# Performance work log

Hardware: AMD Instinct MI355X
Metric: run time of the kernel (lower is better)

The kernel has to match this reference:

```python
import jax, jax.numpy as jnp
import numpy as np

N = 50000
IN_DIM, HID_DIM, OUT_DIM = 16, 64, 32


def setup_inputs() -> dict:
    key = jax.random.key(0)
    k1, k2, k3, k4, k5 = jax.random.split(key, 5)
    x = jax.random.normal(k1, (N, IN_DIM), dtype=jnp.float32)
    edge_index = jax.random.randint(k2, (2, 800000), 0, N, dtype=jnp.int64)
    # GCNConv weights (glorot-ish scale) and biases
    W1 = jax.random.normal(k3, (IN_DIM, HID_DIM), dtype=jnp.float32) / np.sqrt(IN_DIM)
    b1 = jnp.zeros((HID_DIM,), dtype=jnp.float32)
    W2 = jax.random.normal(k4, (HID_DIM, OUT_DIM), dtype=jnp.float32) / np.sqrt(HID_DIM)
    b2 = jnpplus = jnp.zeros((OUT_DIM,), dtype=jnp.float32)
    return {"x": x, "edge_index": edge_index, "W1": W1, "b1": b1, "W2": W2, "b2": b2}


def _gcn_conv(x, src, dst, norm, W, b, num_nodes):
    # PyG GCNConv: h = X W; out[d] = sum_e norm_e * h[src_e]; out += b
    h = x @ W                                   # [N, D_out] small GEMM
    msgs = h[src] * norm[:, None]               # [E+N, D_out] gather (memory-bound)
    out = jax.ops.segment_sum(msgs, dst, num_segments=num_nodes)  # scatter-add
    return out + b


def reference(x, edge_index, W1, b1, W2, b2):
    num_nodes = x.shape[0]
    # add self-loops (PyG GCNConv default add_self_loops=True)
    loops = jnp.arange(num_nodes, dtype=edge_index.dtype)
    src = jnp.concatenate([edge_index[0], loops])
    dst = jnp.concatenate([edge_index[1], loops])
    # symmetric normalization D^{-1/2} (A+I) D^{-1/2}, degree over dst
    deg = jax.ops.segment_sum(jnp.ones_like(src, dtype=x.dtype), dst, num_segments=num_nodes)
    dinv = jnp.where(deg > 0, jax.lax.rsqrt(deg), 0.0)
    norm = dinv[src] * dinv[dst]                # [E+N]

    h = _gcn_conv(x, src, dst, norm, W1, b1, num_nodes)
    h = jax.nn.relu(h)
    out = _gcn_conv(h, src, dst, norm, W2, b2, num_nodes)
    return out
```

## Files before the change

### kernel.cpp

```cpp
#include <hip/hip_runtime.h>
#include <hip/hip_fp16.h>

#define IN_DIM  16
#define HID_DIM 64
#define OUT_DIM 32

#define CAP   8192
#define EPB   1024
#define EPT   4
#define CONVB 64
#define PBT   1024

__device__ __forceinline__ int detect_is64(const void* edges) {
    const int* w = (const int*)edges;
    int is64 = 1;
    #pragma unroll
    for (int i = 0; i < 16; ++i) is64 &= (w[2 * i + 1] == 0);
    return is64;
}

__device__ __forceinline__ long long edge_at(const void* edges, int is64, long long i) {
    if (is64) return ((const long long*)edges)[i];
    return (long long)((const int*)edges)[i];
}

__device__ __forceinline__ int block_incl_scan(int v, int t, int* wsum) {
    int lane = t & 63, w = t >> 6;
    int s = v;
    #pragma unroll
    for (int d = 1; d < 64; d <<= 1) {
        int u = __shfl_up(s, d, 64);
        if (lane >= d) s += u;
    }
    if (lane == 63) wsum[w] = s;
    __syncthreads();
    int add = 0;
    #pragma unroll
    for (int i = 0; i < 4; ++i)
        if (i < w) add += wsum[i];
    return s + add;
}

__global__ __launch_bounds__(256) void k_partA(const void* edges, int* gcur,
                                               unsigned int* gpart, int nbuk, long long E,
                                               const float* __restrict__ x,
                                               __half* __restrict__ xh,
                                               long long xElems, int nblkA) {
    if (blockIdx.x >= nblkA) {
        const float4* x4 = (const float4*)x;
        uint2* outp = (uint2*)xh;
        long long n4 = xElems >> 2;
        for (long long i = (long long)(blockIdx.x - nblkA) * 256 + threadIdx.x;
             i < n4; i += (long long)CONVB * 256) {
            float4 v = x4[i];
            __half2 a = __floats2half2_rn(v.x, v.y);
            __half2 b = __floats2half2_rn(v.z, v.w);
            outp[i] = make_uint2(*(unsigned int*)&a, *(unsigned int*)&b);
        }
        return;
    }

    __shared__ unsigned int staged[EPB];
    __shared__ int hcnt[256], hoff[256], hcur[256];
    __shared__ int wsum[4];
    __shared__ int s64s;
    int t = threadIdx.x;
    if (t == 0) s64s = detect_is64(edges);
    hcnt[t] = 0;
    __syncthreads();
    int is64 = s64s;

    long long e0 = (long long)blockIdx.x * EPB;
    unsigned int rs[EPT], rd[EPT];
    int nval = 0;
    #pragma unroll
    for (int k = 0; k < EPT; ++k) {
        long long e = e0 + t + k * 256;
        if (e < E) {
            rs[k] = (unsigned int)edge_at(edges, is64, e);
            rd[k] = (unsigned int)edge_at(edges, is64, E + e);
            atomicAdd(&hcnt[rd[k] >> 8], 1);
            nval = k + 1;
        }
    }
    __syncthreads();

    int v = hcnt[t];
    int incl = block_incl_scan(v, t, wsum);
    int excl = incl - v;
    hoff[t] = excl;
    hcur[t] = excl;
    __syncthreads();

    #pragma unroll
    for (int k = 0; k < EPT; ++k) {
        if (k < nval) {
            int p = atomicAdd(&hcur[rd[k] >> 8], 1);
            staged[p] = rs[k] | ((rd[k] & 255u) << 16);
        }
    }
    __syncthreads();

    if (t < nbuk) {
        int c = hcnt[t];
        if (c > 0) {
            int base = atomicAdd(&gcur[t], c);
            int o = hoff[t];
            for (int k = 0; k < c; ++k) {
                int idx = base + k;
                if (idx < CAP) gpart[(size_t)t * CAP + idx] = staged[o + k];
            }
        }
    }
}

__global__ __launch_bounds__(PBT) void k_partB(const int* __restrict__ gcur,
                                               const unsigned int* __restrict__ gpart,
                                               unsigned short* __restrict__ csr,
                                               int* __restrict__ offs,
                                               float* __restrict__ dinv,
                                               int nbuk, int N) {
    __shared__ unsigned int   ebuf[CAP];
    __shared__ unsigned short sbuf[CAP];
    __shared__ int bscan[256];
    __shared__ int hcnt[256], hcur[256];
    __shared__ int wsum[4];
    int t = threadIdx.x;
    int lane = t & 63, wv = t >> 6;
    int b = blockIdx.x;

    int bc = (t < 256 && t < nbuk) ? min(gcur[t], CAP) : 0;
    if (t < 256) hcnt[t] = 0;
    int s = bc;
    #pragma unroll
    for (int d = 1; d < 64; d <<= 1) {
        int u = __shfl_up(s, d, 64);
        if (lane >= d) s += u;
    }
    if (t < 256 && lane == 63) wsum[wv] = s;
    __syncthreads();
    if (t < 256) {
        int add = 0;
        #pragma unroll
        for (int i = 0; i < 4; ++i)
            if (i < wv) add += wsum[i];
        bscan[t] = s + add;
    }
    __syncthreads();
    int base = (b == 0) ? 0 : bscan[b - 1];
    int cnt  = bscan[b] - base;

    for (int i = t; i < cnt; i += PBT) ebuf[i] = gpart[(size_t)b * CAP + i];
    __syncthreads();
    for (int i = t; i < cnt; i += PBT) atomicAdd(&hcnt[(ebuf[i] >> 16) & 255u], 1);
    __syncthreads();

    int v = (t < 256) ? hcnt[t] : 0;
    s = v;
    #pragma unroll
    for (int d = 1; d < 64; d <<= 1) {
        int u = __shfl_up(s, d, 64);
        if (lane >= d) s += u;
    }
    if (t < 256 && lane == 63) wsum[wv] = s;
    __syncthreads();
    if (t < 256) {
        int add = 0;
        #pragma unroll
        for (int i = 0; i < 4; ++i)
            if (i < wv) add += wsum[i];
        int excl = (s + add) - v;
        hcur[t] = excl;
        int node = b * 256 + t;
        if (node < N) {
            offs[node] = base + excl;
            dinv[node] = rsqrtf((float)v + 1.0f);
        }
    }
    if (b == nbuk - 1 && t == 0) offs[N] = bscan[nbuk - 1];
    __syncthreads();

    for (int i = t; i < cnt; i += PBT) {
        unsigned int e = ebuf[i];
        int p = atomicAdd(&hcur[(e >> 16) & 255u], 1);
        sbuf[p] = (unsigned short)(e & 0xffffu);
    }
    __syncthreads();
    for (int i = t; i < cnt; i += PBT) csr[base + i] = sbuf[i];
}

#define ASTR 17
#define H1S  68
__global__ __launch_bounds__(256, 6) void k_agg1g(
    const __half* __restrict__ xh, const float* __restrict__ dinv,
    const int* __restrict__ offs, const unsigned short* __restrict__ csr,
    const float* __restrict__ W1, const float* __restrict__ b1,
    const float* __restrict__ W2, __half* __restrict__ h2, int N)
{
    __shared__ __align__(16) float W1s[IN_DIM * HID_DIM];
    __shared__ __align__(16) float W2s[HID_DIM * OUT_DIM];
    __shared__ float b1s[HID_DIM];
    __shared__ __align__(16) float aggs[16 * ASTR];
    __shared__ __align__(16) float h1s[16 * H1S];

    int tid = threadIdx.x;
    int lane = tid & 63;
    int g = lane >> 4, sub = lane & 15;
    int comp = sub >> 3;
    int way  = sub & 7;
    int nl   = (tid >> 6) * 4 + g;
    int node = blockIdx.x * 16 + nl;

    float di = 0.f;
    int start = 0, end = 0;
    if (node < N) {
        di = dinv[node];
        start = offs[node];
        end = offs[node + 1];
    }

    for (int i = tid; i < IN_DIM * HID_DIM; i += 256) W1s[i] = W1[i];
    for (int i = tid; i < HID_DIM * OUT_DIM; i += 256) W2s[i] = W2[i];
    if (tid < HID_DIM) b1s[tid] = b1[tid];

    float acc[8] = {0.f, 0.f, 0.f, 0.f, 0.f, 0.f, 0.f, 0.f};
    if (node < N) {
        const uint4* x2 = (const uint4*)xh;
        if (way == 0) {
            uint4 r = x2[(size_t)node * 2 + comp];
            const __half2* hp = (const __half2*)&r;
            #pragma unroll
            for (int c = 0; c < 4; ++c) {
                float2 f = __half22float2(hp[c]);
                acc[c * 2]     = di * f.x;
                acc[c * 2 + 1] = di * f.y;
            }
        }
        int j = start + way;
        for (; j + 8 < end; j += 16) {
            int s0 = csr[j], s1 = csr[j + 8];
            float w0 = dinv[s0], w1 = dinv[s1];
            uint4 r0 = x2[(size_t)s0 * 2 + comp];
            uint4 r1 = x2[(size_t)s1 * 2 + comp];
            const __half2* hp0 = (const __half2*)&r0;
            const __half2* hp1 = (const __half2*)&r1;
            #pragma unroll
            for (int c = 0; c < 4; ++c) {
                float2 f0 = __half22float2(hp0[c]);
                float2 f1 = __half22float2(hp1[c]);
                acc[c * 2]     += w0 * f0.x + w1 * f1.x;
                acc[c * 2 + 1] += w0 * f0.y + w1 * f1.y;
            }
        }
        if (j < end) {
            int s = csr[j];
            float w = dinv[s];
            uint4 r = x2[(size_t)s * 2 + comp];
            const __half2* hp = (const __half2*)&r;
            #pragma unroll
            for (int c = 0; c < 4; ++c) {
                float2 f = __half22float2(hp[c]);
                acc[c * 2]     += w * f.x;
                acc[c * 2 + 1] += w * f.y;
            }
        }
        #pragma unroll
        for (int m = 1; m <= 4; m <<= 1) {
            #pragma unroll
            for (int c = 0; c < 8; ++c) acc[c] += __shfl_xor(acc[c], m, 64);
        }
    }
    if (way == 0) {
        #pragma unroll
        for (int c = 0; c < 8; ++c) aggs[nl * ASTR + comp * 8 + c] = di * acc[c];
    }
    __syncthreads();

    int nl2 = tid >> 4, q = tid & 15;

    float a1[4];
    #pragma unroll
    for (int c = 0; c < 4; ++c) a1[c] = b1s[q * 4 + c];
    #pragma unroll
    for (int k = 0; k < IN_DIM; ++k) {
        float a = aggs[nl2 * ASTR + k];
        float4 w = *(const float4*)&W1s[k * HID_DIM + q * 4];
        a1[0] += a * w.x; a1[1] += a * w.y; a1[2] += a * w.z; a1[3] += a * w.w;
    }
    *(float4*)&h1s[nl2 * H1S + q * 4] =
        make_float4(fmaxf(a1[0], 0.f), fmaxf(a1[1], 0.f),
                    fmaxf(a1[2], 0.f), fmaxf(a1[3], 0.f));
    __syncthreads();

    float a2x = 0.f, a2y = 0.f;
    const float4* h1row = (const float4*)&h1s[nl2 * H1S];
    #pragma unroll
    for (int k4 = 0; k4 < 16; ++k4) {
        float4 hv = h1row[k4];
        const float* wb = &W2s[(k4 * 4) * OUT_DIM + q * 2];
        float2 w0 = *(const float2*)(wb);
        float2 w1 = *(const float2*)(wb + OUT_DIM);
        float2 w2 = *(const float2*)(wb + 2 * OUT_DIM);
        float2 w3 = *(const float2*)(wb + 3 * OUT_DIM);
        a2x += hv.x * w0.x + hv.y * w1.x + hv.z * w2.x + hv.w * w3.x;
        a2y += hv.x * w0.y + hv.y * w1.y + hv.z * w2.y + hv.w * w3.y;
    }
    int gn = blockIdx.x * 16 + nl2;
    if (gn < N) {
        __half2 p = __floats2half2_rn(a2x, a2y);
        ((unsigned int*)h2)[(size_t)gn * 16 + q] = *(unsigned int*)&p;
    }
}

__global__ __launch_bounds__(256, 8) void k_agg2(
    const __half* __restrict__ h2, const float* __restrict__ dinv,
    const int* __restrict__ offs, const unsigned short* __restrict__ csr,
    const float* __restrict__ b2, float* __restrict__ out, int N)
{
    int gtid = blockIdx.x * 256 + threadIdx.x;
    int lane = gtid & 63;
    int g = lane >> 4, sub = lane & 15;
    int comp = sub & 3, way = sub >> 2;
    int node = (gtid >> 6) * 4 + g;
    if (node >= N) return;
    const uint4* h24 = (const uint4*)h2;
    float di = dinv[node];
    int start = offs[node], end = offs[node + 1];
    float acc[8] = {0.f, 0.f, 0.f, 0.f, 0.f, 0.f, 0.f, 0.f};
    if (way == 0) {
        uint4 r = h24[(size_t)node * 4 + comp];
        const __half2* hp = (const __half2*)&r;
        #pragma unroll
        for (int c = 0; c < 4; ++c) {
            float2 f = __half22float2(hp[c]);
            acc[c * 2]     = di * f.x;
            acc[c * 2 + 1] = di * f.y;
        }
    }
    int j = start + way;
    for (; j + 4 < end; j += 8) {
        int s0 = csr[j], s1 = csr[j + 4];
        float w0 = dinv[s0], w1 = dinv[s1];
        uint4 r0 = h24[(size_t)s0 * 4 + comp];
        uint4 r1 = h24[(size_t)s1 * 4 + comp];
        const __half2* hp0 = (const __half2*)&r0;
        const __half2* hp1 = (const __half2*)&r1;
        #pragma unroll
        for (int c = 0; c < 4; ++c) {
            float2 f0 = __half22float2(hp0[c]);
            float2 f1 = __half22float2(hp1[c]);
            acc[c * 2]     += w0 * f0.x + w1 * f1.x;
            acc[c * 2 + 1] += w0 * f0.y + w1 * f1.y;
        }
    }
    if (j < end) {
        int s = csr[j];
        float w = dinv[s];
        uint4 r = h24[(size_t)s * 4 + comp];
        const __half2* hp = (const __half2*)&r;
        #pragma unroll
        for (int c = 0; c < 4; ++c) {
            float2 f = __half22float2(hp[c]);
            acc[c * 2]     += w * f.x;
            acc[c * 2 + 1] += w * f.y;
        }
    }
    #pragma unroll
    for (int m = 4; m <= 8; m <<= 1) {
        #pragma unroll
        for (int c = 0; c < 8; ++c) acc[c] += __shfl_xor(acc[c], m, 64);
    }
    if (way == 0) {
        const float4* b24 = (const float4*)b2;
        float4 bb0 = b24[comp * 2], bb1 = b24[comp * 2 + 1];
        float4* out4 = (float4*)out;
        out4[(size_t)node * 8 + comp * 2 + 0] =
            make_float4(di * acc[0] + bb0.x, di * acc[1] + bb0.y,
                        di * acc[2] + bb0.z, di * acc[3] + bb0.w);
        out4[(size_t)node * 8 + comp * 2 + 1] =
            make_float4(di * acc[4] + bb1.x, di * acc[5] + bb1.y,
                        di * acc[6] + bb1.z, di * acc[7] + bb1.w);
    }
}

extern "C" void kernel_launch(void* const* d_in, const int* in_sizes, int n_in,
                              void* d_out, int out_size, void* d_ws, size_t ws_size,
                              hipStream_t stream) {
    const float* x     = (const float*)d_in[0];
    const void*  edges = d_in[1];
    const float* W1    = (const float*)d_in[2];
    const float* b1    = (const float*)d_in[3];
    const float* W2    = (const float*)d_in[4];
    const float* b2    = (const float*)d_in[5];
    float* out = (float*)d_out;

    const int       N = in_sizes[0] / IN_DIM;
    const long long E = in_sizes[1] / 2;
    const int    NBUK = (N + 255) >> 8;
    const int   NBLKA = (int)((E + EPB - 1) / EPB);

    unsigned short* csr   = (unsigned short*)d_ws;
    unsigned int*   gpart = (unsigned int*)(csr + ((E + 7) & ~7LL));
    __half* xh       = (__half*)(gpart + (size_t)NBUK * CAP);
    __half* h2       = (__half*)(xh + (size_t)IN_DIM * N);
    float*  dinv     = (float*)(h2 + (size_t)OUT_DIM * N);
    int*    offs     = (int*)(dinv + N);
    int*    gcur     = offs + N + 1;

    const int B = 256;
    hipMemsetAsync(gcur, 0, (size_t)NBUK * sizeof(int), stream);
    k_partA<<<NBLKA + CONVB, B, 0, stream>>>(edges, gcur, gpart, NBUK, E,
                                             x, xh, (long long)N * IN_DIM, NBLKA);
    k_partB<<<NBUK, PBT, 0, stream>>>(gcur, gpart, csr, offs, dinv, NBUK, N);

    k_agg1g<<<(N + 15) / 16, B, 0, stream>>>(xh, dinv, offs, csr,
                                             W1, b1, W2, h2, N);
    k_agg2<<<(N + 15) / 16, B, 0, stream>>>(h2, dinv, offs, csr, b2, out, N);
}
```

Baseline: 143.6 us.

## Store per-block bucket runs contiguously and gather them in partB via histogram

partA now writes its whole locally bucket-sorted edge chunk contiguously and records per-block bucket counts and offsets, instead of doing serialized per-thread scattered writes into global buckets reserved by atomics. A small scan kernel computes the bucket bases, and partB gathers each bucket's runs from every producer block using the per-block histograms. Edges per block rise to 3328 so the number of producer blocks fits the 256-thread scan in partB. The aim is coalesced writes in partA and no per-bucket serial copy loop, at the cost of an extra launch and many short strided reads in partB.

```diff
diff --git a/kernel.cpp b/kernel.cpp
--- a/kernel.cpp
+++ b/kernel.cpp
@@ -5,11 +5,11 @@
 #define HID_DIM 64
 #define OUT_DIM 32
 
-#define CAP   8192
-#define EPB   1024
-#define EPT   4
+#define EPB   3328
+#define EPT   13
 #define CONVB 64
 #define PBT   1024
+#define BCAP  8192
 
 __device__ __forceinline__ int detect_is64(const void* edges) {
     const int* w = (const int*)edges;
@@ -41,8 +41,12 @@
     return s + add;
 }
 
-__global__ __launch_bounds__(256) void k_partA(const void* edges, int* gcur,
-                                               unsigned int* gpart, int nbuk, long long E,
+__global__ __launch_bounds__(256) void k_partA(const void* edges,
+                                               unsigned int* __restrict__ gpart,
+                                               int* __restrict__ H,
+                                               int* __restrict__ Hoff,
+                                               int* __restrict__ tot,
+                                               int nbuk, long long E,
                                                const float* __restrict__ x,
                                                __half* __restrict__ xh,
                                                long long xElems, int nblkA) {
@@ -61,9 +65,9 @@
     }
 
     __shared__ unsigned int staged[EPB];
-    __shared__ int hcnt[256], hoff[256], hcur[256];
+    __shared__ int hcnt[256], hoffs[256], hcur[256];
     __shared__ int wsum[4];
-    __shared__ int s64s;
+    __shared__ int s64s, sTot;
     int t = threadIdx.x;
     if (t == 0) s64s = detect_is64(edges);
     hcnt[t] = 0;
@@ -88,8 +92,9 @@
     int v = hcnt[t];
     int incl = block_incl_scan(v, t, wsum);
     int excl = incl - v;
-    hoff[t] = excl;
+    hoffs[t] = excl;
     hcur[t] = excl;
+    if (t == 255) sTot = incl;
     __syncthreads();
 
     #pragma unroll
@@ -101,37 +106,55 @@
     }
     __syncthreads();
 
+    int nvt = sTot;
+    for (int i = t; i < nvt; i += 256)
+        gpart[(size_t)blockIdx.x * EPB + i] = staged[i];
+
     if (t < nbuk) {
         int c = hcnt[t];
-        if (c > 0) {
-            int base = atomicAdd(&gcur[t], c);
-            int o = hoff[t];
-            for (int k = 0; k < c; ++k) {
-                int idx = base + k;
-                if (idx < CAP) gpart[(size_t)t * CAP + idx] = staged[o + k];
-            }
-        }
-    }
-}
-
-__global__ __launch_bounds__(PBT) void k_partB(const int* __restrict__ gcur,
-                                               const unsigned int* __restrict__ gpart,
+        H[blockIdx.x * nbuk + t]    = c;
+        Hoff[blockIdx.x * nbuk + t] = hoffs[t];
+        if (c > 0) atomicAdd(&tot[t], c);
+    }
+}
+
+__global__ __launch_bounds__(256) void k_scan(const int* __restrict__ tot,
+                                              int* __restrict__ base, int nbuk) {
+    __shared__ int wsum[4];
+    int t = threadIdx.x;
+    int v = (t < nbuk) ? tot[t] : 0;
+    int incl = block_incl_scan(v, t, wsum);
+    if (t < nbuk) base[t] = incl - v;
+    if (t == nbuk - 1) base[nbuk] = incl;
+}
+
+__global__ __launch_bounds__(PBT) void k_partB(const unsigned int* __restrict__ gpart,
+                                               const int* __restrict__ H,
+                                               const int* __restrict__ Hoff,
+                                               const int* __restrict__ base,
                                                unsigned short* __restrict__ csr,
                                                int* __restrict__ offs,
                                                float* __restrict__ dinv,
-                                               int nbuk, int N) {
-    __shared__ unsigned int   ebuf[CAP];
-    __shared__ unsigned short sbuf[CAP];
-    __shared__ int bscan[256];
+                                               int nbuk, int nblkA, int N) {
+    __shared__ unsigned int   ebuf[BCAP];
+    __shared__ unsigned short sbuf[BCAP];
+    __shared__ int runS[256], runC[256], runD[256];
     __shared__ int hcnt[256], hcur[256];
     __shared__ int wsum[4];
+    __shared__ int sTot;
     int t = threadIdx.x;
     int lane = t & 63, wv = t >> 6;
     int b = blockIdx.x;
 
-    int bc = (t < 256 && t < nbuk) ? min(gcur[t], CAP) : 0;
-    if (t < 256) hcnt[t] = 0;
-    int s = bc;
+    int c_i = 0, s_i = 0;
+    if (t < 256) {
+        if (t < nblkA) {
+            c_i = H[t * nbuk + b];
+            s_i = Hoff[t * nbuk + b];
+        }
+        hcnt[t] = 0;
+    }
+    int s = c_i;
     #pragma unroll
     for (int d = 1; d < 64; d <<= 1) {
         int u = __shfl_up(s, d, 64);
@@ -144,14 +167,23 @@
         #pragma unroll
         for (int i = 0; i < 4; ++i)
             if (i < wv) add += wsum[i];
-        bscan[t] = s + add;
-    }
-    __syncthreads();
-    int base = (b == 0) ? 0 : bscan[b - 1];
-    int cnt  = bscan[b] - base;
-
-    for (int i = t; i < cnt; i += PBT) ebuf[i] = gpart[(size_t)b * CAP + i];
-    __syncthreads();
+        int incl = s + add;
+        runD[t] = incl - c_i;
+        runC[t] = c_i;
+        runS[t] = t * EPB + s_i;
+        if (t == 255) sTot = incl;
+    }
+    __syncthreads();
+    int bbase = base[b];
+    int cnt   = sTot;
+
+    for (int r = wv; r < nblkA; r += (PBT / 64)) {
+        int c = runC[r], d0 = runD[r], s0 = runS[r];
+        for (int o = lane; o < c; o += 64)
+            ebuf[d0 + o] = gpart[s0 + o];
+    }
+    __syncthreads();
+
     for (int i = t; i < cnt; i += PBT) atomicAdd(&hcnt[(ebuf[i] >> 16) & 255u], 1);
     __syncthreads();
 
@@ -173,11 +205,11 @@
         hcur[t] = excl;
         int node = b * 256 + t;
         if (node < N) {
-            offs[node] = base + excl;
+            offs[node] = bbase + excl;
             dinv[node] = rsqrtf((float)v + 1.0f);
         }
     }
-    if (b == nbuk - 1 && t == 0) offs[N] = bscan[nbuk - 1];
+    if (b == nbuk - 1 && t == 0) offs[N] = bbase + cnt;
     __syncthreads();
 
     for (int i = t; i < cnt; i += PBT) {
@@ -186,7 +218,7 @@
         sbuf[p] = (unsigned short)(e & 0xffffu);
     }
     __syncthreads();
-    for (int i = t; i < cnt; i += PBT) csr[base + i] = sbuf[i];
+    for (int i = t; i < cnt; i += PBT) csr[bbase + i] = sbuf[i];
 }
 
 #define ASTR 17
@@ -401,17 +433,22 @@
 
     unsigned short* csr   = (unsigned short*)d_ws;
     unsigned int*   gpart = (unsigned int*)(csr + ((E + 7) & ~7LL));
-    __half* xh       = (__half*)(gpart + (size_t)NBUK * CAP);
-    __half* h2       = (__half*)(xh + (size_t)IN_DIM * N);
-    float*  dinv     = (float*)(h2 + (size_t)OUT_DIM * N);
-    int*    offs     = (int*)(dinv + N);
-    int*    gcur     = offs + N + 1;
+    int*    H    = (int*)(gpart + (size_t)NBLKA * EPB);
+    int*    Hoff = H + (size_t)NBLKA * NBUK;
+    int*    tot  = Hoff + (size_t)NBLKA * NBUK;
+    int*    base = tot + NBUK;
+    __half* xh   = (__half*)(base + NBUK + 1);
+    __half* h2   = (__half*)(xh + (size_t)IN_DIM * N);
+    float*  dinv = (float*)(h2 + (size_t)OUT_DIM * N);
+    int*    offs = (int*)(dinv + N);
 
     const int B = 256;
-    hipMemsetAsync(gcur, 0, (size_t)NBUK * sizeof(int), stream);
-    k_partA<<<NBLKA + CONVB, B, 0, stream>>>(edges, gcur, gpart, NBUK, E,
+    hipMemsetAsync(tot, 0, (size_t)NBUK * sizeof(int), stream);
+    k_partA<<<NBLKA + CONVB, B, 0, stream>>>(edges, gpart, H, Hoff, tot, NBUK, E,
                                              x, xh, (long long)N * IN_DIM, NBLKA);
-    k_partB<<<NBUK, PBT, 0, stream>>>(gcur, gpart, csr, offs, dinv, NBUK, N);
+    k_scan<<<1, B, 0, stream>>>(tot, base, NBUK);
+    k_partB<<<NBUK, PBT, 0, stream>>>(gpart, H, Hoff, base, csr, offs, dinv,
+                                      NBUK, NBLKA, N);
 
     k_agg1g<<<(N + 15) / 16, B, 0, stream>>>(xh, dinv, offs, csr,
                                              W1, b1, W2, h2, N);
```

Measured after the change: 134.2 us. -6.6%, faster.

## Enlarge partition blocks to 1024 threads and 3328 edges per block

Applied to the files above, without the earlier changes.

Each partition block of k_partA now uses 1024 threads and handles 3328 edges instead of 256 threads and 1024 edges, and the conversion tail drops from 64 to 16 blocks. The aim is to cut the number of blocks doing global atomic reservations per bucket and to write larger contiguous runs per bucket into gpart. The block scan is rewritten so only the first 256 threads hold histogram bins. The cost is a larger staged shared buffer and fewer, bigger blocks, which may lower occupancy and parallelism.

```diff
diff --git a/kernel.cpp b/kernel.cpp
--- a/kernel.cpp
+++ b/kernel.cpp
@@ -6,9 +6,10 @@
 #define OUT_DIM 32
 
 #define CAP   8192
-#define EPB   1024
+#define EPB   3328
+#define PAT   1024
 #define EPT   4
-#define CONVB 64
+#define CONVB 16
 #define PBT   1024
 
 __device__ __forceinline__ int detect_is64(const void* edges) {
@@ -41,7 +42,7 @@
     return s + add;
 }
 
-__global__ __launch_bounds__(256) void k_partA(const void* edges, int* gcur,
+__global__ __launch_bounds__(PAT) void k_partA(const void* edges, int* gcur,
                                                unsigned int* gpart, int nbuk, long long E,
                                                const float* __restrict__ x,
                                                __half* __restrict__ xh,
@@ -50,8 +51,8 @@
         const float4* x4 = (const float4*)x;
         uint2* outp = (uint2*)xh;
         long long n4 = xElems >> 2;
-        for (long long i = (long long)(blockIdx.x - nblkA) * 256 + threadIdx.x;
-             i < n4; i += (long long)CONVB * 256) {
+        for (long long i = (long long)(blockIdx.x - nblkA) * PAT + threadIdx.x;
+             i < n4; i += (long long)CONVB * PAT) {
             float4 v = x4[i];
             __half2 a = __floats2half2_rn(v.x, v.y);
             __half2 b = __floats2half2_rn(v.z, v.w);
@@ -65,36 +66,51 @@
     __shared__ int wsum[4];
     __shared__ int s64s;
     int t = threadIdx.x;
+    int lane = t & 63, wv = t >> 6;
     if (t == 0) s64s = detect_is64(edges);
-    hcnt[t] = 0;
+    if (t < 256) hcnt[t] = 0;
     __syncthreads();
     int is64 = s64s;
 
     long long e0 = (long long)blockIdx.x * EPB;
     unsigned int rs[EPT], rd[EPT];
-    int nval = 0;
     #pragma unroll
     for (int k = 0; k < EPT; ++k) {
-        long long e = e0 + t + k * 256;
-        if (e < E) {
+        int el = t + k * PAT;
+        long long e = e0 + el;
+        if (el < EPB && e < E) {
             rs[k] = (unsigned int)edge_at(edges, is64, e);
             rd[k] = (unsigned int)edge_at(edges, is64, E + e);
             atomicAdd(&hcnt[rd[k] >> 8], 1);
-            nval = k + 1;
-        }
-    }
-    __syncthreads();
-
-    int v = hcnt[t];
-    int incl = block_incl_scan(v, t, wsum);
-    int excl = incl - v;
-    hoff[t] = excl;
-    hcur[t] = excl;
+        } else {
+            rd[k] = 0xffffffffu;
+        }
+    }
+    __syncthreads();
+
+    int v = (t < 256) ? hcnt[t] : 0;
+    int s = v;
+    #pragma unroll
+    for (int d = 1; d < 64; d <<= 1) {
+        int u = __shfl_up(s, d, 64);
+        if (lane >= d) s += u;
+    }
+    if (t < 256 && lane == 63) wsum[wv] = s;
+    __syncthreads();
+    if (t < 256) {
+        int add = 0;
+        #pragma unroll
+        for (int i = 0; i < 4; ++i)
+            if (i < wv) add += wsum[i];
+        int excl = (s + add) - v;
+        hoff[t] = excl;
+        hcur[t] = excl;
+    }
     __syncthreads();
 
     #pragma unroll
     for (int k = 0; k < EPT; ++k) {
-        if (k < nval) {
+        if (rd[k] != 0xffffffffu) {
             int p = atomicAdd(&hcur[rd[k] >> 8], 1);
             staged[p] = rs[k] | ((rd[k] & 255u) << 16);
         }
@@ -409,8 +425,8 @@
 
     const int B = 256;
     hipMemsetAsync(gcur, 0, (size_t)NBUK * sizeof(int), stream);
-    k_partA<<<NBLKA + CONVB, B, 0, stream>>>(edges, gcur, gpart, NBUK, E,
-                                             x, xh, (long long)N * IN_DIM, NBLKA);
+    k_partA<<<NBLKA + CONVB, PAT, 0, stream>>>(edges, gcur, gpart, NBUK, E,
+                                               x, xh, (long long)N * IN_DIM, NBLKA);
     k_partB<<<NBUK, PBT, 0, stream>>>(gcur, gpart, csr, offs, dinv, NBUK, N);
 
     k_agg1g<<<(N + 15) / 16, B, 0, stream>>>(xh, dinv, offs, csr,
```

Result: faster. 128.9 us (-10.2%).
